# Kernel optimization log

Measured on AMD Instinct MI355X. Metric: run time of the kernel, lower is better.

The kernel has to match this reference:

```python
import jax, jax.numpy as jnp
import numpy as np

M, N, D = 16384, 128, 2048  # actions, question tokens, ExpSet.dim


def setup_inputs() -> dict:
    key = jax.random.key(0)
    ks = jax.random.split(key, 6)
    s1 = 1.0 / np.sqrt(2 * D)  # torch Linear default init bounds
    s2 = 1.0 / np.sqrt(D)
    return {
        "action_embedding": jax.random.normal(ks[0], (M, D), jnp.float32),
        "question_t": jax.random.normal(ks[1], (N, D), jnp.float32),
        "history_t": jax.random.normal(ks[2], (D,), jnp.float32),
        "W1": jax.random.uniform(ks[3], (D, 2 * D), jnp.float32, -s1, s1),
        "b1": jnp.zeros((D,), jnp.float32),
        "W2": jax.random.uniform(ks[4], (D, D), jnp.float32, -s2, s2),
        "b2": jnp.zeros((D,), jnp.float32),
    }


def reference(action_embedding, question_t, history_t, W1, b1, W2, b2):
    # Attention: each action (query) attends over the n question tokens.
    # Equivalent to expand->attend->sum in the torch code, but without
    # materializing the [m, n, d] expanded tensor.
    scores = action_embedding @ question_t.T              # [M, N]
    attn = jax.nn.softmax(scores, axis=1)                 # softmax over tokens
    question = attn @ question_t                          # [M, D] (attended + summed)

    # Perceptron(2d -> d -> d) on cat([history, question])
    hist = jnp.broadcast_to(history_t, (action_embedding.shape[0], history_t.shape[0]))
    qh = jnp.concatenate([hist, question], axis=1)        # [M, 2D]
    h = jax.nn.relu(qh @ W1.T + b1)                       # [M, D]
    qwh = h @ W2.T + b2                                   # [M, D]

    # Elementwise dot with action embeddings, softmax over actions.
    semantic_scores = jnp.sum(qwh * action_embedding, axis=1)  # [M]
    return jax.nn.softmax(semantic_scores, axis=0)
```

## Files before the change

### kernel.cpp

```cpp
#include <hip/hip_runtime.h>
#include <hip/hip_bf16.h>


typedef _Float16 f16;
typedef __attribute__((ext_vector_type(8))) _Float16 half8;
typedef __attribute__((ext_vector_type(4))) _Float16 half4_t;
typedef __attribute__((ext_vector_type(4))) float f32x4;

#define GLL(gp, lp)                                                              \
  __builtin_amdgcn_global_load_lds(                                              \
      (const __attribute__((address_space(1))) void*)(gp),                       \
      (__attribute__((address_space(3))) void*)(lp), 16, 0, 0)

#define WAITN(n)                                                                 \
  do {                                                                           \
    asm volatile("s_waitcnt vmcnt(" #n ")" ::: "memory");                        \
    __builtin_amdgcn_sched_barrier(0);                                           \
  } while (0)

template <int NT, int LDA, int LDB>
__device__ __forceinline__ void kloop1(const f16* __restrict__ A,
                                       const f16* __restrict__ B,
                                       f16* __restrict__ SM,
                                       f32x4 (&acc)[4][4],
                                       int lane, int wv, int wm, int wn) {
  static_assert(NT >= 4, "depth-3 pipeline needs NT >= 4");
  const int f = lane & 15, kk = lane >> 4;
  const int cS = (lane & 7) ^ (lane >> 3);
  const int kkS = (cS & 3) * 8;
  const int rS = 2 * (lane >> 3) + (cS >> 2);
  const size_t offA0 = (size_t)(16 * (wv * 2 + 0) + rS) * LDA + kkS;
  const size_t offA1 = (size_t)(16 * (wv * 2 + 1) + rS) * LDA + kkS;
  const size_t offB0 = (size_t)(16 * (wv * 2 + 0) + rS) * LDB + kkS;
  const size_t offB1 = (size_t)(16 * (wv * 2 + 1) + rS) * LDB + kkS;
  const int Ld0 = (wv * 2 + 0) * 512, Ld1 = (wv * 2 + 1) * 512;

  int aoff[4], boff[4];
  #pragma unroll
  for (int mf = 0; mf < 4; ++mf) {
    const int R = wm + mf * 16 + f;
    const int c2 = (((R & 1) << 2) | kk) ^ ((R >> 1) & 7);
    aoff[mf] = (R >> 1) * 64 + c2 * 8;
  }
  #pragma unroll
  for (int nf = 0; nf < 4; ++nf) {
    const int R = wn + nf * 16 + f;
    const int c2 = (((R & 1) << 2) | kk) ^ ((R >> 1) & 7);
    boff[nf] = (R >> 1) * 64 + c2 * 8;
  }

  auto STAGE = [&](int set, int kt) {
    f16* base = SM + set * 8192;
    GLL(A + offA0 + kt, base + Ld0);
    GLL(A + offA1 + kt, base + Ld1);
    GLL(B + offB0 + kt, base + 4096 + Ld0);
    GLL(B + offB1 + kt, base + 4096 + Ld1);
  };
  auto COMPUTE = [&](int set) {
    const f16* p = SM + set * 8192;
    half8 a[4], b[4];
    #pragma unroll
    for (int mf = 0; mf < 4; ++mf) a[mf] = *(const half8*)&p[aoff[mf]];
    #pragma unroll
    for (int nf = 0; nf < 4; ++nf) b[nf] = *(const half8*)&p[4096 + boff[nf]];
    __builtin_amdgcn_s_setprio(1);
    #pragma unroll
    for (int mf = 0; mf < 4; ++mf)
      #pragma unroll
      for (int nf = 0; nf < 4; ++nf)
        acc[mf][nf] = __builtin_amdgcn_mfma_f32_16x16x32_f16(a[mf], b[nf], acc[mf][nf], 0, 0, 0);
    __builtin_amdgcn_s_setprio(0);
  };

  STAGE(0, 0);
  STAGE(1, 32);
  STAGE(2, 64);
  #pragma unroll 1
  for (int t = 0; t < NT - 3; ++t) {
    STAGE((t + 3) & 3, (t + 3) * 32);
    WAITN(12);
    __builtin_amdgcn_s_barrier();
    COMPUTE(t & 3);
    __builtin_amdgcn_s_barrier();
  }
  WAITN(8);
  __builtin_amdgcn_s_barrier();
  COMPUTE((NT - 3) & 3);
  __builtin_amdgcn_s_barrier();
  WAITN(4);
  __builtin_amdgcn_s_barrier();
  COMPUTE((NT - 2) & 3);
  __builtin_amdgcn_s_barrier();
  WAITN(0);
  __builtin_amdgcn_s_barrier();
  COMPUTE((NT - 1) & 3);
  __builtin_amdgcn_s_barrier();
}

template <int NT, int LDA, int LDB>
__device__ __forceinline__ void kloop256(const f16* __restrict__ A,
                                         const f16* __restrict__ B,
                                         f16* __restrict__ SM,
                                         f32x4 (&acc)[8][4],
                                         int lane, int wv, int wm, int wn) {
  static_assert(NT >= 3, "pipeline needs NT >= 3");
  const int f = lane & 15, kk = lane >> 4;
  const int cS = (lane & 7) ^ (lane >> 3);
  const int kkS = (cS & 3) * 8;
  const int rS = 2 * (lane >> 3) + (cS >> 2);
  const size_t offA0 = (size_t)(16 * (wv * 2 + 0) + rS) * LDA + kkS;
  const size_t offA1 = (size_t)(16 * (wv * 2 + 1) + rS) * LDA + kkS;
  const size_t offB0 = (size_t)(16 * (wv * 2 + 0) + rS) * LDB + kkS;
  const size_t offB1 = (size_t)(16 * (wv * 2 + 1) + rS) * LDB + kkS;
  const int Ld0 = (wv * 2 + 0) * 512, Ld1 = (wv * 2 + 1) * 512;

  int aoff[8], boff[4];
  #pragma unroll
  for (int mf = 0; mf < 8; ++mf) {
    const int R = wm + mf * 16 + f;
    const int c2 = (((R & 1) << 2) | kk) ^ ((R >> 1) & 7);
    aoff[mf] = (R >> 1) * 64 + c2 * 8;
  }
  #pragma unroll
  for (int nf = 0; nf < 4; ++nf) {
    const int R = wn + nf * 16 + f;
    const int c2 = (((R & 1) << 2) | kk) ^ ((R >> 1) & 7);
    boff[nf] = (R >> 1) * 64 + c2 * 8;
  }

  auto STAGE = [&](int set, int kt) {
    f16* base = SM + set * 16384;
    GLL(A + offA0 + kt, base + Ld0);
    GLL(A + offA1 + kt, base + Ld1);
    GLL(B + offB0 + kt, base + 8192 + Ld0);
    GLL(B + offB1 + kt, base + 8192 + Ld1);
  };
  auto COMPUTE = [&](int set) {
    const f16* p = SM + set * 16384;
    half8 a[8], b[4];
    #pragma unroll
    for (int mf = 0; mf < 8; ++mf) a[mf] = *(const half8*)&p[aoff[mf]];
    #pragma unroll
    for (int nf = 0; nf < 4; ++nf) b[nf] = *(const half8*)&p[8192 + boff[nf]];
    __builtin_amdgcn_s_setprio(1);
    #pragma unroll
    for (int mf = 0; mf < 8; ++mf)
      #pragma unroll
      for (int nf = 0; nf < 4; ++nf)
        acc[mf][nf] = __builtin_amdgcn_mfma_f32_16x16x32_f16(a[mf], b[nf], acc[mf][nf], 0, 0, 0);
    __builtin_amdgcn_s_setprio(0);
  };

  STAGE(0, 0);
  STAGE(1, 32);
  #pragma unroll 1
  for (int t = 0; t < NT - 2; ++t) {
    STAGE((t + 2) & 3, (t + 2) * 32);
    WAITN(8);
    __builtin_amdgcn_s_barrier();
    COMPUTE(t & 3);
  }
  WAITN(4);
  __builtin_amdgcn_s_barrier();
  COMPUTE((NT - 2) & 3);
  WAITN(0);
  __builtin_amdgcn_s_barrier();
  COMPUTE((NT - 1) & 3);
}


__global__ __launch_bounds__(256) void c_kernel(const float* __restrict__ W1,
                                                const float* __restrict__ b1,
                                                const float* __restrict__ hist,
                                                float* __restrict__ c) {
  const int wave = threadIdx.x >> 6, lane = threadIdx.x & 63;
  const int j = blockIdx.x * 4 + wave;
  const float* row = W1 + (size_t)j * 4096;
  float s = 0.f;
  #pragma unroll 2
  for (int kq = lane; kq < 512; kq += 64) {
    const float4 w = *(const float4*)&row[kq * 4];
    const float4 h = *(const float4*)&hist[kq * 4];
    s += w.x * h.x + w.y * h.y + w.z * h.z + w.w * h.w;
  }
  #pragma unroll
  for (int mask = 1; mask < 64; mask <<= 1) s += __shfl_xor(s, mask);
  if (lane == 0) c[j] = s + b1[j];
}

__device__ __forceinline__ half4_t f16hi4(const float4 v) {
  half4_t h;
  h.x = (f16)v.x; h.y = (f16)v.y; h.z = (f16)v.z; h.w = (f16)v.w;
  return h;
}

__global__ __launch_bounds__(256) void prep_AQ(const float* __restrict__ A,
                                               const float* __restrict__ Q,
                                               const float* __restrict__ b2,
                                               f16* __restrict__ Af,
                                               f16* __restrict__ Qf,
                                               float* __restrict__ ab2) {
  const int wv = threadIdx.x >> 6, lane = threadIdx.x & 63;
  if (blockIdx.x < 4096) {
    const size_t row = (size_t)blockIdx.x * 4 + wv;
    const float* ar = A + row * 2048;
    float dot = 0.f;
    #pragma unroll 2
    for (int c0 = 0; c0 < 2048; c0 += 256) {
      const int col = c0 + lane * 4;
      const float4 v = *(const float4*)&ar[col];
      const float4 bb = *(const float4*)&b2[col];
      dot += v.x * bb.x + v.y * bb.y + v.z * bb.z + v.w * bb.w;
      *(half4_t*)&Af[row * 2048 + col] = f16hi4(v);
    }
    #pragma unroll
    for (int mask = 1; mask < 64; mask <<= 1) dot += __shfl_xor(dot, mask);
    if (lane == 0) ab2[row] = dot;
  } else {
    const size_t row = (size_t)(blockIdx.x - 4096) * 4 + wv;
    const float* qr = Q + row * 2048;
    #pragma unroll 2
    for (int c0 = 0; c0 < 2048; c0 += 256) {
      const int col = c0 + lane * 4;
      const float4 v = *(const float4*)&qr[col];
      *(half4_t*)&Qf[row * 2048 + col] = f16hi4(v);
    }
  }
}

__global__ __launch_bounds__(256) void transpose_f16(const float* __restrict__ src,
                                                     int R, int C,
                                                     f16* __restrict__ dst) {
  __shared__ float T[64][65];
  const int c0 = blockIdx.x * 64, r0 = blockIdx.y * 64;
  const int t = threadIdx.x;
  {
    const int rl = t >> 4, cl = (t & 15) * 4;
    #pragma unroll
    for (int ii = 0; ii < 4; ++ii) {
      const float4 v = *(const float4*)&src[(size_t)(r0 + rl + ii * 16) * C + c0 + cl];
      T[rl + ii * 16][cl + 0] = v.x; T[rl + ii * 16][cl + 1] = v.y;
      T[rl + ii * 16][cl + 2] = v.z; T[rl + ii * 16][cl + 3] = v.w;
    }
  }
  __syncthreads();
  const int cc = t >> 2, rr0 = (t & 3) * 16;
  f16 u[16];
  #pragma unroll
  for (int k = 0; k < 16; ++k) u[k] = (f16)T[rr0 + k][cc];
  f16* ph = dst + (size_t)(c0 + cc) * R + r0 + rr0;
  #pragma unroll
  for (int k4 = 0; k4 < 4; ++k4)
    *(half4_t*)&ph[k4 * 4] = *(half4_t*)&u[k4 * 4];
}

template <int BM, int TM>
__global__ __launch_bounds__(256) void gemm_bt_sk(const float* __restrict__ A,
                                                  const float* __restrict__ B,
                                                  float* __restrict__ Cpart,
                                                  int Kslab, int lda, int ldb,
                                                  int ldc, int M) {
  constexpr int BN = 64, BK = 32;
  constexpr int ASTR = BM + 12, BSTR = BN + 4;
  __shared__ float As[BK][ASTR];
  __shared__ float Bs[BK][BSTR];
  const int tid = threadIdx.x;
  const int tx = tid & 15, ty = tid >> 4;
  const int m0 = ty * TM, n0 = tx * 4;
  const size_t bm = (size_t)blockIdx.x * BM, bn = (size_t)blockIdx.y * BN;
  const int kb = blockIdx.z * Kslab;
  const float* Ab = A + bm * lda;
  const float* Bb = B + bn * ldb;
  float acc[TM][4];
  #pragma unroll
  for (int i = 0; i < TM; ++i)
    #pragma unroll
    for (int j = 0; j < 4; ++j) acc[i][j] = 0.f;
  for (int kt = kb; kt < kb + Kslab; kt += BK) {
    #pragma unroll
    for (int it = 0; it < BM * BK / 4 / 256; ++it) {
      const int idx = it * 256 + tid;
      const int row = idx >> 3, kq = idx & 7;
      const float4 v = *(const float4*)&Ab[(size_t)row * lda + kt + kq * 4];
      As[kq * 4 + 0][row] = v.x; As[kq * 4 + 1][row] = v.y;
      As[kq * 4 + 2][row] = v.z; As[kq * 4 + 3][row] = v.w;
    }
    #pragma unroll
    for (int it = 0; it < BN * BK / 4 / 256; ++it) {
      const int idx = it * 256 + tid;
      const int row = idx >> 3, kq = idx & 7;
      const float4 v = *(const float4*)&Bb[(size_t)row * ldb + kt + kq * 4];
      Bs[kq * 4 + 0][row] = v.x; Bs[kq * 4 + 1][row] = v.y;
      Bs[kq * 4 + 2][row] = v.z; Bs[kq * 4 + 3][row] = v.w;
    }
    __syncthreads();
    #pragma unroll
    for (int k = 0; k < BK; ++k) {
      float av[TM];
      #pragma unroll
      for (int i = 0; i < TM; ++i) av[i] = As[k][m0 + i];
      const float4 b = *(const float4*)&Bs[k][n0];
      const float bv[4] = {b.x, b.y, b.z, b.w};
      #pragma unroll
      for (int i = 0; i < TM; ++i)
        #pragma unroll
        for (int j = 0; j < 4; ++j) acc[i][j] = fmaf(av[i], bv[j], acc[i][j]);
    }
    __syncthreads();
  }
  float* base = Cpart + (size_t)blockIdx.z * M * ldc;
  #pragma unroll
  for (int i = 0; i < TM; ++i) {
    float* crow = base + (bm + m0 + i) * (size_t)ldc + bn + n0;
    #pragma unroll
    for (int j = 0; j < 4; ++j) crow[j] = acc[i][j];
  }
}

__global__ __launch_bounds__(256) void qwt_combine(const float* __restrict__ part,
                                                   f16* __restrict__ QWt) {
  const size_t i = ((size_t)blockIdx.x * 256 + threadIdx.x) * 4;
  float4 s = make_float4(0.f, 0.f, 0.f, 0.f);
  #pragma unroll
  for (int z = 0; z < 8; ++z) {
    const float4 v = *(const float4*)&part[(size_t)z * 262144 + i];
    s.x += v.x; s.y += v.y; s.z += v.z; s.w += v.w;
  }
  *(half4_t*)&QWt[i] = f16hi4(s);
}

__global__ __launch_bounds__(256, 2) void s_attn(const f16* __restrict__ Af,
                                                 const f16* __restrict__ Qf,
                                                 f16* __restrict__ at) {
  __shared__ f16 SM[32768];
  const int tid = threadIdx.x, lane = tid & 63, wv = tid >> 6;
  const int wm = (wv >> 1) * 64, wn = (wv & 1) * 64;
  const int f = lane & 15, kk = lane >> 4;
  const size_t bm = (size_t)blockIdx.x * 128;

  f32x4 acc[4][4];
  #pragma unroll
  for (int mf = 0; mf < 4; ++mf)
    #pragma unroll
    for (int nf = 0; nf < 4; ++nf) acc[mf][nf] = 0.f;

  kloop1<64, 2048, 2048>(Af + bm * 2048, Qf, SM, acc, lane, wv, wm, wn);

  float* sred = (float*)SM;
  float* ssum = sred + 256;
  const int rowbase = wm + kk * 4;
  float rmax[4][4];
  #pragma unroll
  for (int mf = 0; mf < 4; ++mf)
    #pragma unroll
    for (int r = 0; r < 4; ++r) {
      float m4 = fmaxf(fmaxf(acc[mf][0][r], acc[mf][1][r]),
                       fmaxf(acc[mf][2][r], acc[mf][3][r]));
      m4 = fmaxf(m4, __shfl_xor(m4, 1));
      m4 = fmaxf(m4, __shfl_xor(m4, 2));
      m4 = fmaxf(m4, __shfl_xor(m4, 4));
      m4 = fmaxf(m4, __shfl_xor(m4, 8));
      rmax[mf][r] = m4;
    }
  if (f == 0) {
    #pragma unroll
    for (int mf = 0; mf < 4; ++mf)
      #pragma unroll
      for (int r = 0; r < 4; ++r)
        sred[(rowbase + mf * 16 + r) * 2 + (wv & 1)] = rmax[mf][r];
  }
  __syncthreads();
  #pragma unroll
  for (int mf = 0; mf < 4; ++mf)
    #pragma unroll
    for (int r = 0; r < 4; ++r) {
      const int row = rowbase + mf * 16 + r;
      rmax[mf][r] = fmaxf(sred[row * 2], sred[row * 2 + 1]);
    }
  float rsum[4][4];
  #pragma unroll
  for (int mf = 0; mf < 4; ++mf)
    #pragma unroll
    for (int r = 0; r < 4; ++r) {
      float s = 0.f;
      #pragma unroll
      for (int nf = 0; nf < 4; ++nf) {
        acc[mf][nf][r] = __expf(acc[mf][nf][r] - rmax[mf][r]);
        s += acc[mf][nf][r];
      }
      s += __shfl_xor(s, 1);
      s += __shfl_xor(s, 2);
      s += __shfl_xor(s, 4);
      s += __shfl_xor(s, 8);
      rsum[mf][r] = s;
    }
  if (f == 0) {
    #pragma unroll
    for (int mf = 0; mf < 4; ++mf)
      #pragma unroll
      for (int r = 0; r < 4; ++r)
        ssum[(rowbase + mf * 16 + r) * 2 + (wv & 1)] = rsum[mf][r];
  }
  __syncthreads();
  #pragma unroll
  for (int mf = 0; mf < 4; ++mf)
    #pragma unroll
    for (int r = 0; r < 4; ++r) {
      const int row = rowbase + mf * 16 + r;
      const float inv = 1.0f / (ssum[row * 2] + ssum[row * 2 + 1]);
      const size_t orow = (bm + row) * 128;
      #pragma unroll
      for (int nf = 0; nf < 4; ++nf)
        at[orow + wn + nf * 16 + f] = (f16)(acc[mf][nf][r] * inv);
    }
}

__global__ __launch_bounds__(256, 2) void h_kernel(const f16* __restrict__ at,
                                                   const f16* __restrict__ QWt,
                                                   const float* __restrict__ cvec,
                                                   f16* __restrict__ H) {
  __shared__ f16 SM[32768];
  const int tid = threadIdx.x, lane = tid & 63, wv = tid >> 6;
  const int wm = (wv >> 1) * 64, wn = (wv & 1) * 64;
  const int f = lane & 15, kk = lane >> 4;
  const size_t bm = (size_t)(blockIdx.x & 127) * 128;
  const size_t bn = (size_t)(blockIdx.x >> 7) * 128;

  f32x4 acc[4][4];
  #pragma unroll
  for (int mf = 0; mf < 4; ++mf)
    #pragma unroll
    for (int nf = 0; nf < 4; ++nf) acc[mf][nf] = 0.f;

  kloop1<4, 128, 128>(at + bm * 128, QWt + bn * 128, SM, acc, lane, wv, wm, wn);

  float ccv[4];
  #pragma unroll
  for (int nf = 0; nf < 4; ++nf) ccv[nf] = cvec[bn + wn + nf * 16 + f];
  #pragma unroll
  for (int mf = 0; mf < 4; ++mf)
    #pragma unroll
    for (int r = 0; r < 4; ++r) {
      const size_t row = bm + wm + mf * 16 + kk * 4 + r;
      #pragma unroll
      for (int nf = 0; nf < 4; ++nf)
        H[row * 2048 + bn + wn + nf * 16 + f] =
            (f16)fmaxf(acc[mf][nf][r] + ccv[nf], 0.f);
    }
}

__global__ __launch_bounds__(512, 1) void fused_g(
    const f16* __restrict__ Af, const f16* __restrict__ H,
    const f16* __restrict__ W2t, float* __restrict__ partial) {
  extern __shared__ f16 SM[];
  const int tid = threadIdx.x, lane = tid & 63, wv = tid >> 6;
  const int wm = (wv >> 2) * 128, wn = (wv & 3) * 64;
  const int f = lane & 15, kk = lane >> 4;
  const int lin = blockIdx.x;
  const int sid = (lin & 7) * 64 + (lin >> 3);
  const int bmI = sid & 63, bnI = sid >> 6;
  const size_t bm = (size_t)bmI * 256;
  const size_t bn = (size_t)bnI * 256;

  f32x4 acc[8][4];
  #pragma unroll
  for (int mf = 0; mf < 8; ++mf)
    #pragma unroll
    for (int nf = 0; nf < 4; ++nf) acc[mf][nf] = 0.f;

  kloop256<64, 2048, 2048>(Af + bm * 2048, W2t + bn * 2048, SM, acc, lane, wv, wm, wn);

  float part[8][4];
  #pragma unroll
  for (int mf = 0; mf < 8; ++mf)
    #pragma unroll
    for (int r = 0; r < 4; ++r) {
      const size_t hrow = (bm + wm + mf * 16 + kk * 4 + r) * 2048 + bn + wn + f;
      float s = 0.f;
      #pragma unroll
      for (int nf = 0; nf < 4; ++nf)
        s += (float)H[hrow + nf * 16] * acc[mf][nf][r];
      part[mf][r] = s;
    }
  #pragma unroll
  for (int mf = 0; mf < 8; ++mf)
    #pragma unroll
    for (int r = 0; r < 4; ++r) {
      part[mf][r] += __shfl_xor(part[mf][r], 1);
      part[mf][r] += __shfl_xor(part[mf][r], 2);
      part[mf][r] += __shfl_xor(part[mf][r], 4);
      part[mf][r] += __shfl_xor(part[mf][r], 8);
    }
  if (f == 0) {
    const size_t slab = (size_t)(bnI * 4 + (wv & 3)) * 16384;
    #pragma unroll
    for (int mf = 0; mf < 8; ++mf)
      #pragma unroll
      for (int r = 0; r < 4; ++r)
        partial[slab + bm + wm + mf * 16 + kk * 4 + r] = part[mf][r];
  }
}


__global__ __launch_bounds__(256) void k_sem(const float* __restrict__ partial,
                                             const float* __restrict__ ab2,
                                             float* __restrict__ semantic,
                                             float* __restrict__ bstats) {
  const int m = blockIdx.x * 256 + threadIdx.x;
  float s = ab2[m];
  #pragma unroll
  for (int nb = 0; nb < 32; ++nb) s += partial[(size_t)nb * 16384 + m];
  semantic[m] = s;
  float mx = s;
  #pragma unroll
  for (int mask = 1; mask < 64; mask <<= 1) mx = fmaxf(mx, __shfl_xor(mx, mask));
  __shared__ float wmax[4], wsum[4];
  const int wave = threadIdx.x >> 6, lane = threadIdx.x & 63;
  if (lane == 0) wmax[wave] = mx;
  __syncthreads();
  const float bmax = fmaxf(fmaxf(wmax[0], wmax[1]), fmaxf(wmax[2], wmax[3]));
  float e = expf(s - bmax);
  #pragma unroll
  for (int mask = 1; mask < 64; mask <<= 1) e += __shfl_xor(e, mask);
  if (lane == 0) wsum[wave] = e;
  __syncthreads();
  if (threadIdx.x == 0) {
    bstats[blockIdx.x * 2] = bmax;
    bstats[blockIdx.x * 2 + 1] = wsum[0] + wsum[1] + wsum[2] + wsum[3];
  }
}

__global__ __launch_bounds__(256) void k_out(const float* __restrict__ semantic,
                                             const float* __restrict__ bstats,
                                             float* __restrict__ out) {
  __shared__ float g0s, g1s;
  const int tid = threadIdx.x;
  if (tid < 64) {
    const float bm = bstats[tid * 2], bs = bstats[tid * 2 + 1];
    float gm = bm;
    #pragma unroll
    for (int mask = 1; mask < 64; mask <<= 1) gm = fmaxf(gm, __shfl_xor(gm, mask));
    float gs = bs * expf(bm - gm);
    #pragma unroll
    for (int mask = 1; mask < 64; mask <<= 1) gs += __shfl_xor(gs, mask);
    if (tid == 0) { g0s = gm; g1s = gs; }
  }
  __syncthreads();
  const int m = blockIdx.x * 256 + tid;
  out[m] = expf(semantic[m] - g0s) / g1s;
}


extern "C" void kernel_launch(void* const* d_in, const int* in_sizes, int n_in,
                              void* d_out, int out_size, void* d_ws, size_t ws_size,
                              hipStream_t stream) {
  (void)in_sizes; (void)n_in; (void)out_size; (void)ws_size;
  const float* A    = (const float*)d_in[0];
  const float* Q    = (const float*)d_in[1];
  const float* hist = (const float*)d_in[2];
  const float* W1   = (const float*)d_in[3];
  const float* b1   = (const float*)d_in[4];
  const float* W2   = (const float*)d_in[5];
  const float* b2   = (const float*)d_in[6];
  float* out = (float*)d_out;

  char* ws = (char*)d_ws;
  f16* Af      = (f16*)ws;   ws += (size_t)16384 * 2048 * 2;
  f16* Hbuf    = (f16*)ws;   ws += (size_t)16384 * 2048 * 2;
  f16* W2t     = (f16*)ws;   ws += (size_t)2048 * 2048 * 2;
  f16* Qf      = (f16*)ws;   ws += (size_t)128 * 2048 * 2;
  f16* QWt     = (f16*)ws;   ws += (size_t)2048 * 128 * 2;
  f16* at      = (f16*)ws;   ws += (size_t)16384 * 128 * 2;
  float* qwt_part = (float*)ws; ws += (size_t)8 * 2048 * 128 * 4;
  float* c_vec = (float*)ws; ws += 2048 * 4;
  float* ab2   = (float*)ws; ws += 16384 * 4;
  float* partial  = (float*)ws; ws += (size_t)32 * 16384 * 4;
  float* semantic = (float*)ws; ws += 16384 * 4;
  float* bstats   = (float*)ws; ws += 128 * 4;

  hipFuncSetAttribute((const void*)fused_g,
                      hipFuncAttributeMaxDynamicSharedMemorySize, 131072);

  c_kernel<<<512, 256, 0, stream>>>(W1, b1, hist, c_vec);
  gemm_bt_sk<32, 2><<<dim3(64, 2, 8), 256, 0, stream>>>(W1 + 2048, Q, qwt_part,
                                                        256, 4096, 2048, 128, 2048);
  qwt_combine<<<256, 256, 0, stream>>>(qwt_part, QWt);
  transpose_f16<<<dim3(32, 32), 256, 0, stream>>>(W2, 2048, 2048, W2t);
  prep_AQ<<<4128, 256, 0, stream>>>(A, Q, b2, Af, Qf, ab2);
  s_attn<<<128, 256, 0, stream>>>(Af, Qf, at);
  h_kernel<<<2048, 256, 0, stream>>>(at, QWt, c_vec, Hbuf);
  fused_g<<<512, 512, 131072, stream>>>(Af, Hbuf, W2t, partial);
  k_sem<<<64, 256, 0, stream>>>(partial, ab2, semantic, bstats);
  k_out<<<64, 256, 0, stream>>>(semantic, bstats, out);
}
```

Measured before the change: 272.4 us.

## Shrink fused_g tile to 256x128 with 3-stage LDS ring for two blocks per CU

The main W2 GEMM kernel moves from 256x256 tiles (each wave holding 8x4 accumulators) to 256x128 tiles (4x4 per wave), launching twice as many blocks. The LDS pipeline goes from four 32KB stages to three 24KB stages, so shared memory drops to 72KB and launch bounds allow two blocks per CU. A second barrier after each compute step guards reuse of the three-slot ring. The aim is higher occupancy and better latency hiding, traded against more A-tile reloads and an extra barrier per k-step.

```diff
diff --git a/kernel.cpp b/kernel.cpp
--- a/kernel.cpp
+++ b/kernel.cpp
@@ -98,11 +98,11 @@
 }
 
 template <int NT, int LDA, int LDB>
-__device__ __forceinline__ void kloop256(const f16* __restrict__ A,
-                                         const f16* __restrict__ B,
-                                         f16* __restrict__ SM,
-                                         f32x4 (&acc)[8][4],
-                                         int lane, int wv, int wm, int wn) {
+__device__ __forceinline__ void kloopG(const f16* __restrict__ A,
+                                       const f16* __restrict__ B,
+                                       f16* __restrict__ SM,
+                                       f32x4 (&acc)[4][4],
+                                       int lane, int wv, int wm, int wn) {
   static_assert(NT >= 3, "pipeline needs NT >= 3");
   const int f = lane & 15, kk = lane >> 4;
   const int cS = (lane & 7) ^ (lane >> 3);
@@ -110,13 +110,13 @@
   const int rS = 2 * (lane >> 3) + (cS >> 2);
   const size_t offA0 = (size_t)(16 * (wv * 2 + 0) + rS) * LDA + kkS;
   const size_t offA1 = (size_t)(16 * (wv * 2 + 1) + rS) * LDA + kkS;
-  const size_t offB0 = (size_t)(16 * (wv * 2 + 0) + rS) * LDB + kkS;
-  const size_t offB1 = (size_t)(16 * (wv * 2 + 1) + rS) * LDB + kkS;
-  const int Ld0 = (wv * 2 + 0) * 512, Ld1 = (wv * 2 + 1) * 512;
-
-  int aoff[8], boff[4];
-  #pragma unroll
-  for (int mf = 0; mf < 8; ++mf) {
+  const size_t offB0 = (size_t)(16 * wv + rS) * LDB + kkS;
+  const int LdA0 = (wv * 2 + 0) * 512, LdA1 = (wv * 2 + 1) * 512;
+  const int LdB0 = 8192 + wv * 512;
+
+  int aoff[4], boff[4];
+  #pragma unroll
+  for (int mf = 0; mf < 4; ++mf) {
     const int R = wm + mf * 16 + f;
     const int c2 = (((R & 1) << 2) | kk) ^ ((R >> 1) & 7);
     aoff[mf] = (R >> 1) * 64 + c2 * 8;
@@ -125,26 +125,25 @@
   for (int nf = 0; nf < 4; ++nf) {
     const int R = wn + nf * 16 + f;
     const int c2 = (((R & 1) << 2) | kk) ^ ((R >> 1) & 7);
-    boff[nf] = (R >> 1) * 64 + c2 * 8;
+    boff[nf] = 8192 + (R >> 1) * 64 + c2 * 8;
   }
 
   auto STAGE = [&](int set, int kt) {
-    f16* base = SM + set * 16384;
-    GLL(A + offA0 + kt, base + Ld0);
-    GLL(A + offA1 + kt, base + Ld1);
-    GLL(B + offB0 + kt, base + 8192 + Ld0);
-    GLL(B + offB1 + kt, base + 8192 + Ld1);
+    f16* base = SM + set * 12288;
+    GLL(A + offA0 + kt, base + LdA0);
+    GLL(A + offA1 + kt, base + LdA1);
+    GLL(B + offB0 + kt, base + LdB0);
   };
   auto COMPUTE = [&](int set) {
-    const f16* p = SM + set * 16384;
-    half8 a[8], b[4];
-    #pragma unroll
-    for (int mf = 0; mf < 8; ++mf) a[mf] = *(const half8*)&p[aoff[mf]];
-    #pragma unroll
-    for (int nf = 0; nf < 4; ++nf) b[nf] = *(const half8*)&p[8192 + boff[nf]];
+    const f16* p = SM + set * 12288;
+    half8 a[4], b[4];
+    #pragma unroll
+    for (int mf = 0; mf < 4; ++mf) a[mf] = *(const half8*)&p[aoff[mf]];
+    #pragma unroll
+    for (int nf = 0; nf < 4; ++nf) b[nf] = *(const half8*)&p[boff[nf]];
     __builtin_amdgcn_s_setprio(1);
     #pragma unroll
-    for (int mf = 0; mf < 8; ++mf)
+    for (int mf = 0; mf < 4; ++mf)
       #pragma unroll
       for (int nf = 0; nf < 4; ++nf)
         acc[mf][nf] = __builtin_amdgcn_mfma_f32_16x16x32_f16(a[mf], b[nf], acc[mf][nf], 0, 0, 0);
@@ -153,19 +152,25 @@
 
   STAGE(0, 0);
   STAGE(1, 32);
+  int cs = 0;
   #pragma unroll 1
   for (int t = 0; t < NT - 2; ++t) {
-    STAGE((t + 2) & 3, (t + 2) * 32);
-    WAITN(8);
+    int ss = cs + 2; if (ss >= 3) ss -= 3;
+    STAGE(ss, (t + 2) * 32);
+    WAITN(6);
     __builtin_amdgcn_s_barrier();
-    COMPUTE(t & 3);
-  }
-  WAITN(4);
-  __builtin_amdgcn_s_barrier();
-  COMPUTE((NT - 2) & 3);
+    COMPUTE(cs);
+    __builtin_amdgcn_s_barrier();
+    ++cs; if (cs == 3) cs = 0;
+  }
+  WAITN(3);
+  __builtin_amdgcn_s_barrier();
+  COMPUTE(cs);
+  __builtin_amdgcn_s_barrier();
+  ++cs; if (cs == 3) cs = 0;
   WAITN(0);
   __builtin_amdgcn_s_barrier();
-  COMPUTE((NT - 1) & 3);
+  COMPUTE(cs);
 }
 
 
@@ -449,30 +454,30 @@
     }
 }
 
-__global__ __launch_bounds__(512, 1) void fused_g(
+__global__ __launch_bounds__(512, 2) void fused_g(
     const f16* __restrict__ Af, const f16* __restrict__ H,
     const f16* __restrict__ W2t, float* __restrict__ partial) {
   extern __shared__ f16 SM[];
   const int tid = threadIdx.x, lane = tid & 63, wv = tid >> 6;
-  const int wm = (wv >> 2) * 128, wn = (wv & 3) * 64;
+  const int wm = (wv >> 1) * 64, wn = (wv & 1) * 64;
   const int f = lane & 15, kk = lane >> 4;
   const int lin = blockIdx.x;
-  const int sid = (lin & 7) * 64 + (lin >> 3);
+  const int sid = (lin & 7) * 128 + (lin >> 3);
   const int bmI = sid & 63, bnI = sid >> 6;
   const size_t bm = (size_t)bmI * 256;
-  const size_t bn = (size_t)bnI * 256;
-
-  f32x4 acc[8][4];
-  #pragma unroll
-  for (int mf = 0; mf < 8; ++mf)
+  const size_t bn = (size_t)bnI * 128;
+
+  f32x4 acc[4][4];
+  #pragma unroll
+  for (int mf = 0; mf < 4; ++mf)
     #pragma unroll
     for (int nf = 0; nf < 4; ++nf) acc[mf][nf] = 0.f;
 
-  kloop256<64, 2048, 2048>(Af + bm * 2048, W2t + bn * 2048, SM, acc, lane, wv, wm, wn);
-
-  float part[8][4];
-  #pragma unroll
-  for (int mf = 0; mf < 8; ++mf)
+  kloopG<64, 2048, 2048>(Af + bm * 2048, W2t + bn * 2048, SM, acc, lane, wv, wm, wn);
+
+  float part[4][4];
+  #pragma unroll
+  for (int mf = 0; mf < 4; ++mf)
     #pragma unroll
     for (int r = 0; r < 4; ++r) {
       const size_t hrow = (bm + wm + mf * 16 + kk * 4 + r) * 2048 + bn + wn + f;
@@ -483,7 +488,7 @@
       part[mf][r] = s;
     }
   #pragma unroll
-  for (int mf = 0; mf < 8; ++mf)
+  for (int mf = 0; mf < 4; ++mf)
     #pragma unroll
     for (int r = 0; r < 4; ++r) {
       part[mf][r] += __shfl_xor(part[mf][r], 1);
@@ -492,9 +497,9 @@
       part[mf][r] += __shfl_xor(part[mf][r], 8);
     }
   if (f == 0) {
-    const size_t slab = (size_t)(bnI * 4 + (wv & 3)) * 16384;
-    #pragma unroll
-    for (int mf = 0; mf < 8; ++mf)
+    const size_t slab = (size_t)(bnI * 2 + (wv & 1)) * 16384;
+    #pragma unroll
+    for (int mf = 0; mf < 4; ++mf)
       #pragma unroll
       for (int r = 0; r < 4; ++r)
         partial[slab + bm + wm + mf * 16 + kk * 4 + r] = part[mf][r];
@@ -579,7 +584,7 @@
   float* bstats   = (float*)ws; ws += 128 * 4;
 
   hipFuncSetAttribute((const void*)fused_g,
-                      hipFuncAttributeMaxDynamicSharedMemorySize, 131072);
+                      hipFuncAttributeMaxDynamicSharedMemorySize, 73728);
 
   c_kernel<<<512, 256, 0, stream>>>(W1, b1, hist, c_vec);
   gemm_bt_sk<32, 2><<<dim3(64, 2, 8), 256, 0, stream>>>(W1 + 2048, Q, qwt_part,
@@ -589,7 +594,7 @@
   prep_AQ<<<4128, 256, 0, stream>>>(A, Q, b2, Af, Qf, ab2);
   s_attn<<<128, 256, 0, stream>>>(Af, Qf, at);
   h_kernel<<<2048, 256, 0, stream>>>(at, QWt, c_vec, Hbuf);
-  fused_g<<<512, 512, 131072, stream>>>(Af, Hbuf, W2t, partial);
+  fused_g<<<1024, 512, 73728, stream>>>(Af, Hbuf, W2t, partial);
   k_sem<<<64, 256, 0, stream>>>(partial, ab2, semantic, bstats);
   k_out<<<64, 256, 0, stream>>>(semantic, bstats, out);
 }
```

Result: slower. 297.0 us (+9.1%).

## Interleave LDS reads, global prefetch and MFMA in four phases per k-step

Applied to the files above, without the earlier changes.

Restructures the 256x256 GEMM k-loop so each k-step is split into four phases. Each phase issues a subset of LDS fragment reads and one global-to-LDS prefetch, then runs a quarter of the MFMAs, with a barrier between phases. The aim is to spread memory issue across the compute and hide LDS latency behind MFMA work, in a ping-pong style schedule. In exchange it adds more barriers and lgkmcnt(0) waits per k-step, which could stall waves.

```diff
diff --git a/kernel.cpp b/kernel.cpp
--- a/kernel.cpp
+++ b/kernel.cpp
@@ -17,6 +17,14 @@
     asm volatile("s_waitcnt vmcnt(" #n ")" ::: "memory");                        \
     __builtin_amdgcn_sched_barrier(0);                                           \
   } while (0)
+
+#define LGKM0                                                                    \
+  do {                                                                           \
+    asm volatile("s_waitcnt lgkmcnt(0)" ::: "memory");                           \
+    __builtin_amdgcn_sched_barrier(0);                                           \
+  } while (0)
+
+#define MFMA16(a, b, c) __builtin_amdgcn_mfma_f32_16x16x32_f16(a, b, c, 0, 0, 0)
 
 template <int NT, int LDA, int LDB>
 __device__ __forceinline__ void kloop1(const f16* __restrict__ A,
@@ -68,7 +76,7 @@
     for (int mf = 0; mf < 4; ++mf)
       #pragma unroll
       for (int nf = 0; nf < 4; ++nf)
-        acc[mf][nf] = __builtin_amdgcn_mfma_f32_16x16x32_f16(a[mf], b[nf], acc[mf][nf], 0, 0, 0);
+        acc[mf][nf] = MFMA16(a[mf], b[nf], acc[mf][nf]);
     __builtin_amdgcn_s_setprio(0);
   };
 
@@ -98,11 +106,11 @@
 }
 
 template <int NT, int LDA, int LDB>
-__device__ __forceinline__ void kloop256(const f16* __restrict__ A,
-                                         const f16* __restrict__ B,
-                                         f16* __restrict__ SM,
-                                         f32x4 (&acc)[8][4],
-                                         int lane, int wv, int wm, int wn) {
+__device__ __forceinline__ void kloop256p(const f16* __restrict__ A,
+                                          const f16* __restrict__ B,
+                                          f16* __restrict__ SM,
+                                          f32x4 (&acc)[8][4],
+                                          int lane, int wv, int wm, int wn) {
   static_assert(NT >= 3, "pipeline needs NT >= 3");
   const int f = lane & 15, kk = lane >> 4;
   const int cS = (lane & 7) ^ (lane >> 3);
@@ -125,47 +133,86 @@
   for (int nf = 0; nf < 4; ++nf) {
     const int R = wn + nf * 16 + f;
     const int c2 = (((R & 1) << 2) | kk) ^ ((R >> 1) & 7);
-    boff[nf] = (R >> 1) * 64 + c2 * 8;
-  }
-
-  auto STAGE = [&](int set, int kt) {
-    f16* base = SM + set * 16384;
-    GLL(A + offA0 + kt, base + Ld0);
-    GLL(A + offA1 + kt, base + Ld1);
-    GLL(B + offB0 + kt, base + 8192 + Ld0);
-    GLL(B + offB1 + kt, base + 8192 + Ld1);
+    boff[nf] = 8192 + (R >> 1) * 64 + c2 * 8;
+  }
+
+  auto PHASES = [&](int cs, int ts, int kt2, bool stage) {
+    const f16* p = SM + cs * 16384;
+    f16* sb = SM + ts * 16384;
+    half8 a[8], b[4];
+    #pragma unroll
+    for (int mf = 0; mf < 4; ++mf) a[mf] = *(const half8*)&p[aoff[mf]];
+    b[0] = *(const half8*)&p[boff[0]];
+    b[1] = *(const half8*)&p[boff[1]];
+    if (stage) GLL(A + offA0 + kt2, sb + Ld0);
+    LGKM0;
+    __builtin_amdgcn_s_setprio(1);
+    #pragma unroll
+    for (int mf = 0; mf < 4; ++mf)
+      #pragma unroll
+      for (int nf = 0; nf < 2; ++nf)
+        acc[mf][nf] = MFMA16(a[mf], b[nf], acc[mf][nf]);
+    __builtin_amdgcn_s_setprio(0);
+    __builtin_amdgcn_s_barrier();
+    #pragma unroll
+    for (int mf = 4; mf < 8; ++mf) a[mf] = *(const half8*)&p[aoff[mf]];
+    if (stage) GLL(A + offA1 + kt2, sb + Ld1);
+    LGKM0;
+    __builtin_amdgcn_s_setprio(1);
+    #pragma unroll
+    for (int mf = 4; mf < 8; ++mf)
+      #pragma unroll
+      for (int nf = 0; nf < 2; ++nf)
+        acc[mf][nf] = MFMA16(a[mf], b[nf], acc[mf][nf]);
+    __builtin_amdgcn_s_setprio(0);
+    __builtin_amdgcn_s_barrier();
+    b[2] = *(const half8*)&p[boff[2]];
+    b[3] = *(const half8*)&p[boff[3]];
+    if (stage) GLL(B + offB0 + kt2, sb + 8192 + Ld0);
+    LGKM0;
+    __builtin_amdgcn_s_setprio(1);
+    #pragma unroll
+    for (int mf = 0; mf < 4; ++mf)
+      #pragma unroll
+      for (int nf = 2; nf < 4; ++nf)
+        acc[mf][nf] = MFMA16(a[mf], b[nf], acc[mf][nf]);
+    __builtin_amdgcn_s_setprio(0);
+    __builtin_amdgcn_s_barrier();
+    if (stage) GLL(B + offB1 + kt2, sb + 8192 + Ld1);
+    __builtin_amdgcn_s_setprio(1);
+    #pragma unroll
+    for (int mf = 4; mf < 8; ++mf)
+      #pragma unroll
+      for (int nf = 2; nf < 4; ++nf)
+        acc[mf][nf] = MFMA16(a[mf], b[nf], acc[mf][nf]);
+    __builtin_amdgcn_s_setprio(0);
+    __builtin_amdgcn_s_barrier();
   };
-  auto COMPUTE = [&](int set) {
-    const f16* p = SM + set * 16384;
-    half8 a[8], b[4];
-    #pragma unroll
-    for (int mf = 0; mf < 8; ++mf) a[mf] = *(const half8*)&p[aoff[mf]];
-    #pragma unroll
-    for (int nf = 0; nf < 4; ++nf) b[nf] = *(const half8*)&p[8192 + boff[nf]];
-    __builtin_amdgcn_s_setprio(1);
-    #pragma unroll
-    for (int mf = 0; mf < 8; ++mf)
-      #pragma unroll
-      for (int nf = 0; nf < 4; ++nf)
-        acc[mf][nf] = __builtin_amdgcn_mfma_f32_16x16x32_f16(a[mf], b[nf], acc[mf][nf], 0, 0, 0);
-    __builtin_amdgcn_s_setprio(0);
-  };
-
-  STAGE(0, 0);
-  STAGE(1, 32);
+
+  {
+    f16* s0 = SM;
+    f16* s1 = SM + 16384;
+    GLL(A + offA0, s0 + Ld0);
+    GLL(A + offA1, s0 + Ld1);
+    GLL(B + offB0, s0 + 8192 + Ld0);
+    GLL(B + offB1, s0 + 8192 + Ld1);
+    GLL(A + offA0 + 32, s1 + Ld0);
+    GLL(A + offA1 + 32, s1 + Ld1);
+    GLL(B + offB0 + 32, s1 + 8192 + Ld0);
+    GLL(B + offB1 + 32, s1 + 8192 + Ld1);
+  }
   #pragma unroll 1
   for (int t = 0; t < NT - 2; ++t) {
-    STAGE((t + 2) & 3, (t + 2) * 32);
-    WAITN(8);
+    WAITN(4);
     __builtin_amdgcn_s_barrier();
-    COMPUTE(t & 3);
+    PHASES(t & 3, (t + 2) & 3, (t + 2) * 32, true);
   }
   WAITN(4);
   __builtin_amdgcn_s_barrier();
-  COMPUTE((NT - 2) & 3);
+  PHASES((NT - 2) & 3, 0, 0, false);
   WAITN(0);
   __builtin_amdgcn_s_barrier();
-  COMPUTE((NT - 1) & 3);
+  PHASES((NT - 1) & 3, 0, 0, false);
 }
 
 
@@ -468,7 +515,7 @@
     #pragma unroll
     for (int nf = 0; nf < 4; ++nf) acc[mf][nf] = 0.f;
 
-  kloop256<64, 2048, 2048>(Af + bm * 2048, W2t + bn * 2048, SM, acc, lane, wv, wm, wn);
+  kloop256p<64, 2048, 2048>(Af + bm * 2048, W2t + bn * 2048, SM, acc, lane, wv, wm, wn);
 
   float part[8][4];
   #pragma unroll
```

Measured after the change: 273.3 us. No clear change (+0.3%).

## Split-K the attention score GEMM and stage h_kernel output through LDS

Applied to the files above, without the earlier changes.

The attention score GEMM now runs as a 2-way split-K over 256 blocks instead of 128. On a GPU with 256 CUs this roughly doubles occupancy for that stage. Partial fp32 scores go to a new workspace buffer, and a separate softmax_at kernel sums the two halves, applies the row softmax and writes fp16 attention weights. h_kernel now stages its ReLU output tile in shared memory so it can write H with 16-byte coalesced stores instead of scattered 2-byte stores. The costs are an extra kernel launch and an 8 MB fp32 round trip for the partial scores. The B-offset constant is also folded into boff.

```diff
diff --git a/kernel.cpp b/kernel.cpp
--- a/kernel.cpp
+++ b/kernel.cpp
@@ -17,6 +17,8 @@
     asm volatile("s_waitcnt vmcnt(" #n ")" ::: "memory");                        \
     __builtin_amdgcn_sched_barrier(0);                                           \
   } while (0)
+
+#define MFMA16(a, b, c) __builtin_amdgcn_mfma_f32_16x16x32_f16(a, b, c, 0, 0, 0)
 
 template <int NT, int LDA, int LDB>
 __device__ __forceinline__ void kloop1(const f16* __restrict__ A,
@@ -68,7 +70,7 @@
     for (int mf = 0; mf < 4; ++mf)
       #pragma unroll
       for (int nf = 0; nf < 4; ++nf)
-        acc[mf][nf] = __builtin_amdgcn_mfma_f32_16x16x32_f16(a[mf], b[nf], acc[mf][nf], 0, 0, 0);
+        acc[mf][nf] = MFMA16(a[mf], b[nf], acc[mf][nf]);
     __builtin_amdgcn_s_setprio(0);
   };
 
@@ -125,7 +127,7 @@
   for (int nf = 0; nf < 4; ++nf) {
     const int R = wn + nf * 16 + f;
     const int c2 = (((R & 1) << 2) | kk) ^ ((R >> 1) & 7);
-    boff[nf] = (R >> 1) * 64 + c2 * 8;
+    boff[nf] = 8192 + (R >> 1) * 64 + c2 * 8;
   }
 
   auto STAGE = [&](int set, int kt) {
@@ -141,13 +143,13 @@
     #pragma unroll
     for (int mf = 0; mf < 8; ++mf) a[mf] = *(const half8*)&p[aoff[mf]];
     #pragma unroll
-    for (int nf = 0; nf < 4; ++nf) b[nf] = *(const half8*)&p[8192 + boff[nf]];
+    for (int nf = 0; nf < 4; ++nf) b[nf] = *(const half8*)&p[boff[nf]];
     __builtin_amdgcn_s_setprio(1);
     #pragma unroll
     for (int mf = 0; mf < 8; ++mf)
       #pragma unroll
       for (int nf = 0; nf < 4; ++nf)
-        acc[mf][nf] = __builtin_amdgcn_mfma_f32_16x16x32_f16(a[mf], b[nf], acc[mf][nf], 0, 0, 0);
+        acc[mf][nf] = MFMA16(a[mf], b[nf], acc[mf][nf]);
     __builtin_amdgcn_s_setprio(0);
   };
 
@@ -329,14 +331,15 @@
   *(half4_t*)&QWt[i] = f16hi4(s);
 }
 
-__global__ __launch_bounds__(256, 2) void s_attn(const f16* __restrict__ Af,
-                                                 const f16* __restrict__ Qf,
-                                                 f16* __restrict__ at) {
+__global__ __launch_bounds__(256, 2) void s_attn_sk(const f16* __restrict__ Af,
+                                                    const f16* __restrict__ Qf,
+                                                    float* __restrict__ Sp) {
   __shared__ f16 SM[32768];
   const int tid = threadIdx.x, lane = tid & 63, wv = tid >> 6;
   const int wm = (wv >> 1) * 64, wn = (wv & 1) * 64;
   const int f = lane & 15, kk = lane >> 4;
-  const size_t bm = (size_t)blockIdx.x * 128;
+  const size_t bm = (size_t)(blockIdx.x >> 1) * 128;
+  const int kz = blockIdx.x & 1;
 
   f32x4 acc[4][4];
   #pragma unroll
@@ -344,75 +347,57 @@
     #pragma unroll
     for (int nf = 0; nf < 4; ++nf) acc[mf][nf] = 0.f;
 
-  kloop1<64, 2048, 2048>(Af + bm * 2048, Qf, SM, acc, lane, wv, wm, wn);
-
-  float* sred = (float*)SM;
-  float* ssum = sred + 256;
-  const int rowbase = wm + kk * 4;
-  float rmax[4][4];
+  kloop1<32, 2048, 2048>(Af + bm * 2048 + kz * 1024, Qf + kz * 1024,
+                         SM, acc, lane, wv, wm, wn);
+
+  float* out = Sp + (size_t)kz * 16384 * 128;
   #pragma unroll
   for (int mf = 0; mf < 4; ++mf)
     #pragma unroll
     for (int r = 0; r < 4; ++r) {
-      float m4 = fmaxf(fmaxf(acc[mf][0][r], acc[mf][1][r]),
-                       fmaxf(acc[mf][2][r], acc[mf][3][r]));
-      m4 = fmaxf(m4, __shfl_xor(m4, 1));
-      m4 = fmaxf(m4, __shfl_xor(m4, 2));
-      m4 = fmaxf(m4, __shfl_xor(m4, 4));
-      m4 = fmaxf(m4, __shfl_xor(m4, 8));
-      rmax[mf][r] = m4;
-    }
-  if (f == 0) {
-    #pragma unroll
-    for (int mf = 0; mf < 4; ++mf)
-      #pragma unroll
-      for (int r = 0; r < 4; ++r)
-        sred[(rowbase + mf * 16 + r) * 2 + (wv & 1)] = rmax[mf][r];
-  }
-  __syncthreads();
-  #pragma unroll
-  for (int mf = 0; mf < 4; ++mf)
-    #pragma unroll
-    for (int r = 0; r < 4; ++r) {
-      const int row = rowbase + mf * 16 + r;
-      rmax[mf][r] = fmaxf(sred[row * 2], sred[row * 2 + 1]);
-    }
-  float rsum[4][4];
-  #pragma unroll
-  for (int mf = 0; mf < 4; ++mf)
-    #pragma unroll
-    for (int r = 0; r < 4; ++r) {
-      float s = 0.f;
-      #pragma unroll
-      for (int nf = 0; nf < 4; ++nf) {
-        acc[mf][nf][r] = __expf(acc[mf][nf][r] - rmax[mf][r]);
-        s += acc[mf][nf][r];
-      }
-      s += __shfl_xor(s, 1);
-      s += __shfl_xor(s, 2);
-      s += __shfl_xor(s, 4);
-      s += __shfl_xor(s, 8);
-      rsum[mf][r] = s;
-    }
-  if (f == 0) {
-    #pragma unroll
-    for (int mf = 0; mf < 4; ++mf)
-      #pragma unroll
-      for (int r = 0; r < 4; ++r)
-        ssum[(rowbase + mf * 16 + r) * 2 + (wv & 1)] = rsum[mf][r];
-  }
-  __syncthreads();
-  #pragma unroll
-  for (int mf = 0; mf < 4; ++mf)
-    #pragma unroll
-    for (int r = 0; r < 4; ++r) {
-      const int row = rowbase + mf * 16 + r;
-      const float inv = 1.0f / (ssum[row * 2] + ssum[row * 2 + 1]);
-      const size_t orow = (bm + row) * 128;
+      const size_t row = bm + wm + mf * 16 + kk * 4 + r;
       #pragma unroll
       for (int nf = 0; nf < 4; ++nf)
-        at[orow + wn + nf * 16 + f] = (f16)(acc[mf][nf][r] * inv);
-    }
+        out[row * 128 + wn + nf * 16 + f] = acc[mf][nf][r];
+    }
+}
+
+__global__ __launch_bounds__(256) void softmax_at(const float* __restrict__ Sp,
+                                                  f16* __restrict__ at) {
+  const int tid = threadIdx.x;
+  const int sub = tid & 7;
+  const size_t row = (size_t)blockIdx.x * 32 + (tid >> 3);
+  const float* p0 = Sp + row * 128 + sub * 16;
+  const float* p1 = p0 + (size_t)16384 * 128;
+  float v[16];
+  #pragma unroll
+  for (int q = 0; q < 4; ++q) {
+    const float4 a = ((const float4*)p0)[q];
+    const float4 b = ((const float4*)p1)[q];
+    v[q * 4 + 0] = a.x + b.x; v[q * 4 + 1] = a.y + b.y;
+    v[q * 4 + 2] = a.z + b.z; v[q * 4 + 3] = a.w + b.w;
+  }
+  float mx = v[0];
+  #pragma unroll
+  for (int e = 1; e < 16; ++e) mx = fmaxf(mx, v[e]);
+  mx = fmaxf(mx, __shfl_xor(mx, 1));
+  mx = fmaxf(mx, __shfl_xor(mx, 2));
+  mx = fmaxf(mx, __shfl_xor(mx, 4));
+  float sm = 0.f;
+  #pragma unroll
+  for (int e = 0; e < 16; ++e) { v[e] = __expf(v[e] - mx); sm += v[e]; }
+  sm += __shfl_xor(sm, 1);
+  sm += __shfl_xor(sm, 2);
+  sm += __shfl_xor(sm, 4);
+  const float inv = 1.0f / sm;
+  f16* po = at + row * 128 + sub * 16;
+  #pragma unroll
+  for (int q = 0; q < 4; ++q) {
+    half4_t h;
+    h.x = (f16)(v[q * 4 + 0] * inv); h.y = (f16)(v[q * 4 + 1] * inv);
+    h.z = (f16)(v[q * 4 + 2] * inv); h.w = (f16)(v[q * 4 + 3] * inv);
+    *(half4_t*)&po[q * 4] = h;
+  }
 }
 
 __global__ __launch_bounds__(256, 2) void h_kernel(const f16* __restrict__ at,
@@ -437,16 +422,28 @@
   float ccv[4];
   #pragma unroll
   for (int nf = 0; nf < 4; ++nf) ccv[nf] = cvec[bn + wn + nf * 16 + f];
+
+  __syncthreads();
+  constexpr int STR = 136;
+  f16* T = SM;
   #pragma unroll
   for (int mf = 0; mf < 4; ++mf)
     #pragma unroll
     for (int r = 0; r < 4; ++r) {
-      const size_t row = bm + wm + mf * 16 + kk * 4 + r;
+      const int row = wm + mf * 16 + kk * 4 + r;
       #pragma unroll
       for (int nf = 0; nf < 4; ++nf)
-        H[row * 2048 + bn + wn + nf * 16 + f] =
+        T[row * STR + wn + nf * 16 + f] =
             (f16)fmaxf(acc[mf][nf][r] + ccv[nf], 0.f);
     }
+  __syncthreads();
+  #pragma unroll
+  for (int it = 0; it < 8; ++it) {
+    const int row = it * 16 + (tid >> 4);
+    const int ch = tid & 15;
+    const float4 vv = *(const float4*)&T[row * STR + ch * 8];
+    *(float4*)&H[(bm + row) * 2048 + bn + ch * 8] = vv;
+  }
 }
 
 __global__ __launch_bounds__(512, 1) void fused_g(
@@ -572,6 +569,7 @@
   f16* QWt     = (f16*)ws;   ws += (size_t)2048 * 128 * 2;
   f16* at      = (f16*)ws;   ws += (size_t)16384 * 128 * 2;
   float* qwt_part = (float*)ws; ws += (size_t)8 * 2048 * 128 * 4;
+  float* Sp    = (float*)ws; ws += (size_t)2 * 16384 * 128 * 4;
   float* c_vec = (float*)ws; ws += 2048 * 4;
   float* ab2   = (float*)ws; ws += 16384 * 4;
   float* partial  = (float*)ws; ws += (size_t)32 * 16384 * 4;
@@ -587,7 +585,8 @@
   qwt_combine<<<256, 256, 0, stream>>>(qwt_part, QWt);
   transpose_f16<<<dim3(32, 32), 256, 0, stream>>>(W2, 2048, 2048, W2t);
   prep_AQ<<<4128, 256, 0, stream>>>(A, Q, b2, Af, Qf, ab2);
-  s_attn<<<128, 256, 0, stream>>>(Af, Qf, at);
+  s_attn_sk<<<256, 256, 0, stream>>>(Af, Qf, Sp);
+  softmax_at<<<512, 256, 0, stream>>>(Sp, at);
   h_kernel<<<2048, 256, 0, stream>>>(at, QWt, c_vec, Hbuf);
   fused_g<<<512, 512, 131072, stream>>>(Af, Hbuf, W2t, partial);
   k_sem<<<64, 256, 0, stream>>>(partial, ab2, semantic, bstats);
```

Measured after the change: 269.7 us (median of 3 runs). No clear change (-1.0%).
